# Kernel tuning notes

Hardware: AMD Instinct MI355X
Metric: run time of the kernel (lower is better)

The kernel has to match this reference:

```python
import jax, jax.numpy as jnp
import numpy as np


def setup_inputs() -> dict:
    key = jax.random.key(0)
    k1, k2 = jax.random.split(key)
    B, S, H, D = 2, 2048, 16, 64
    qk = jax.random.normal(k1, (B, S, 2, H, D), dtype=jnp.float32)
    v = jax.random.normal(k2, (B, S, H, D), dtype=jnp.float32)
    return {"qk": qk, "v": v}


def reference(qk, v):
    # qk: (B, S, 2, H, D); v: (B, S, H, D)
    seqlen = qk.shape[1]
    q = qk[:, :, 0]  # (B, S, H, D)
    k = qk[:, :, 1]
    # elu(x) + 1 feature map (positive features)
    q = jax.nn.elu(q) + 1.0
    k = jax.nn.elu(k) + 1.0
    # explicit O(S^2) score matrix: (B, H, T, S)
    scores = jnp.einsum('bthd,bshd->bhts', q, k)
    mask = jnp.tril(jnp.ones((seqlen, seqlen), dtype=scores.dtype))
    scores = scores * mask
    nu = scores.sum(axis=-1)  # (B, H, T)
    attention = scores / nu[:, :, :, None]
    # dropout_p = 0.0 (eval mode): identity
    output = jnp.einsum('bhts,bshd->bthd', attention, v)
    return output
```

## Files before the change

kernel.cpp:

```cpp
#include <hip/hip_runtime.h>


#define BB 2
#define SS 2048
#define HH 16
#define DD 64
#define CC 128
#define NC (SS / CC)
#define BH (BB * HH)
#define NCHUNK (BH * NC)
#define STSZ (DD * DD + DD)

#define WS_KB (512LL * 4160 * 4)
#define WS_VT (WS_KB + 512LL * 16384)
#define WS_S0 (WS_VT + 512LL * 16384)
#define WS_KZ (WS_S0 + 512LL * 8192)

typedef __attribute__((ext_vector_type(8))) short bf16x8;
typedef __attribute__((ext_vector_type(4))) float f32x4;

__device__ __forceinline__ float phi(float x) {
    return x > 0.f ? x + 1.f : __expf(x);
}
__device__ __forceinline__ unsigned short f2bf(float x) {
    unsigned int u = __float_as_uint(x);
    u += 0x7fffu + ((u >> 16) & 1u);
    return (unsigned short)(u >> 16);
}
__device__ __forceinline__ float bf2f(unsigned short b) {
    return __uint_as_float(((unsigned int)b) << 16);
}
__device__ __forceinline__ void gload16(const void* g, void* lds) {
    __builtin_amdgcn_global_load_lds(
        (const __attribute__((address_space(1))) unsigned int*)g,
        (__attribute__((address_space(3))) unsigned int*)lds, 16, 0, 0);
}

__global__ __launch_bounds__(256, 2)
void prep_state(const float* __restrict__ qk, const float* __restrict__ v,
                float* __restrict__ st, unsigned short* __restrict__ kbg,
                unsigned short* __restrict__ vtg) {
    __shared__ unsigned short Kt[DD][136];
    __shared__ unsigned short Vt[DD][136];

    const int tid = threadIdx.x, blk = blockIdx.x;
    const int bh = blk / NC, c = blk % NC, b = bh / HH, h = bh % HH;
    const int s0 = c * CC;
    const int lr = tid >> 4, lc = (tid & 15) * 4;
    char* kbc = (char*)kbg + (size_t)blk * 16384;

    #pragma unroll
    for (int it = 0; it < 8; ++it) {
        int row = it * 16 + lr;
        size_t ka = ((size_t)((b * SS + s0 + row) * 2 + 1)) * (HH * DD) + h * DD + lc;
        float4 kv = *(const float4*)(qk + ka);
        unsigned short k0 = f2bf(phi(kv.x)), k1 = f2bf(phi(kv.y));
        unsigned short k2 = f2bf(phi(kv.z)), k3 = f2bf(phi(kv.w));
        *(ushort4*)(kbc + row * 128 + ((lc * 2) ^ ((row & 7) << 4))) = make_ushort4(k0, k1, k2, k3);
        Kt[lc + 0][row] = k0; Kt[lc + 1][row] = k1;
        Kt[lc + 2][row] = k2; Kt[lc + 3][row] = k3;
        size_t va = ((size_t)((b * SS + s0 + row) * HH + h)) * DD + lc;
        float4 vv = *(const float4*)(v + va);
        Vt[lc + 0][row] = f2bf(vv.x); Vt[lc + 1][row] = f2bf(vv.y);
        Vt[lc + 2][row] = f2bf(vv.z); Vt[lc + 3][row] = f2bf(vv.w);
    }
    __syncthreads();

    {
        char* vtc = (char*)vtg + (size_t)blk * 16384;
        int e = tid >> 2, sq = (tid & 3) * 32;
        #pragma unroll
        for (int k8 = 0; k8 < 4; ++k8) {
            int s = sq + k8 * 8;
            bf16x8 val = *(const bf16x8*)&Vt[e][s];
            *(bf16x8*)(vtc + e * 256 + ((s * 2) ^ ((e & 7) << 4))) = val;
        }
    }

    const int w = tid >> 6, lane = tid & 63, g = lane >> 4, ln = lane & 15;
    bf16x8 av[4];
    #pragma unroll
    for (int ks = 0; ks < 4; ++ks)
        av[ks] = *(const bf16x8*)&Vt[w * 16 + ln][ks * 32 + g * 8];
    bf16x8 ones;
    #pragma unroll
    for (int j = 0; j < 8; ++j) ones[j] = (short)0x3F80;

    float* stc = st + (size_t)blk * STSZ;
    #pragma unroll
    for (int n = 0; n < 4; ++n) {
        f32x4 a = {0.f, 0.f, 0.f, 0.f}, kz4 = {0.f, 0.f, 0.f, 0.f};
        #pragma unroll
        for (int ks = 0; ks < 4; ++ks) {
            bf16x8 bk = *(const bf16x8*)&Kt[n * 16 + ln][ks * 32 + g * 8];
            a = __builtin_amdgcn_mfma_f32_16x16x32_bf16(av[ks], bk, a, 0, 0, 0);
            kz4 = __builtin_amdgcn_mfma_f32_16x16x32_bf16(ones, bk, kz4, 0, 0, 0);
        }
        #pragma unroll
        for (int r = 0; r < 4; ++r)
            stc[(w * 16 + g * 4 + r) * 64 + n * 16 + ln] = a[r];
        if (w == 0 && g == 0) stc[4096 + n * 16 + ln] = kz4[0];
    }
}

__global__ __launch_bounds__(256)
void chunk_scan(const float* __restrict__ st, unsigned short* __restrict__ s0g,
                float* __restrict__ kzg) {
    int flat = blockIdx.x * 256 + threadIdx.x;
    int bh = flat / 1040, i = flat % 1040;
    if (i < 1024) {
        int i4 = i * 4;
        int e = i4 >> 6, d = i4 & 63;
        const float* src = st + (size_t)(bh * NC) * STSZ + i4;
        char* dst = (char*)s0g + (size_t)(bh * NC) * 8192
                    + e * 128 + ((d * 2) ^ ((e & 7) << 4));
        float4 run = {0.f, 0.f, 0.f, 0.f};
        #pragma unroll
        for (int c2 = 0; c2 < NC; ++c2) {
            *(ushort4*)(dst + (size_t)c2 * 8192) =
                make_ushort4(f2bf(run.x), f2bf(run.y), f2bf(run.z), f2bf(run.w));
            float4 x = *(const float4*)(src + (size_t)c2 * STSZ);
            run.x += x.x; run.y += x.y; run.z += x.z; run.w += x.w;
        }
    } else {
        int j = (i - 1024) * 4;
        const float* src = st + (size_t)(bh * NC) * STSZ + 4096 + j;
        float* dst = kzg + (size_t)(bh * NC) * 64 + j;
        float4 run = {0.f, 0.f, 0.f, 0.f};
        #pragma unroll
        for (int c2 = 0; c2 < NC; ++c2) {
            *(float4*)(dst + (size_t)c2 * 64) = run;
            float4 x = *(const float4*)(src + (size_t)c2 * STSZ);
            run.x += x.x; run.y += x.y; run.z += x.z; run.w += x.w;
        }
    }
}

__global__ __launch_bounds__(256, 2)
void lin_attn_out(const float* __restrict__ qk,
                  const unsigned short* __restrict__ kbg,
                  const unsigned short* __restrict__ vtg,
                  const unsigned short* __restrict__ s0g,
                  const float* __restrict__ kzg,
                  float* __restrict__ out) {
    __shared__ __align__(16) char KbL[16384];
    __shared__ __align__(16) char VtL[16384];
    __shared__ __align__(16) char S0L[8192];
    __shared__ float kzl[DD];
    __shared__ __align__(16) unsigned short Wl[4][32][40];
    __shared__ float nul[4][32];

    const int tid = threadIdx.x, blk = blockIdx.x;
    const int bh = blk / NC, c = blk % NC, b = bh / HH, h = bh % HH;
    const int s0 = c * CC;
    const int w = tid >> 6, lane = tid & 63, g = lane >> 4, ln = lane & 15;

    {
        const char* kbs = (const char*)kbg + (size_t)blk * 16384;
        const char* vts = (const char*)vtg + (size_t)blk * 16384;
        const char* s0s = (const char*)s0g + (size_t)blk * 8192;
        #pragma unroll
        for (int i = 0; i < 4; ++i) {
            gload16(kbs + w * 4096 + i * 1024 + lane * 16, KbL + w * 4096 + i * 1024);
            gload16(vts + w * 4096 + i * 1024 + lane * 16, VtL + w * 4096 + i * 1024);
        }
        #pragma unroll
        for (int i = 0; i < 2; ++i)
            gload16(s0s + w * 2048 + i * 1024 + lane * 16, S0L + w * 2048 + i * 1024);
        if (tid < DD) kzl[tid] = kzg[(size_t)blk * 64 + tid];
    }

    bf16x8 aq[2][2];
    #pragma unroll
    for (int m = 0; m < 2; ++m) {
        int tg = s0 + w * 32 + m * 16 + ln;
        const float* qrow = qk + ((size_t)((b * SS + tg) * 2)) * (HH * DD) + h * DD;
        #pragma unroll
        for (int kb2 = 0; kb2 < 2; ++kb2) {
            float4 x0 = *(const float4*)(qrow + kb2 * 32 + g * 8);
            float4 x1 = *(const float4*)(qrow + kb2 * 32 + g * 8 + 4);
            bf16x8 f;
            f[0] = (short)f2bf(phi(x0.x)); f[1] = (short)f2bf(phi(x0.y));
            f[2] = (short)f2bf(phi(x0.z)); f[3] = (short)f2bf(phi(x0.w));
            f[4] = (short)f2bf(phi(x1.x)); f[5] = (short)f2bf(phi(x1.y));
            f[6] = (short)f2bf(phi(x1.z)); f[7] = (short)f2bf(phi(x1.w));
            aq[m][kb2] = f;
        }
    }
    __syncthreads();

    f32x4 O[2][4];
    #pragma unroll
    for (int m = 0; m < 2; ++m)
        #pragma unroll
        for (int n = 0; n < 4; ++n) O[m][n] = (f32x4){0.f, 0.f, 0.f, 0.f};

    #pragma unroll
    for (int n = 0; n < 4; ++n) {
        int e = n * 16 + ln;
        bf16x8 b0 = *(const bf16x8*)(S0L + e * 128 + ((g * 16) ^ ((e & 7) << 4)));
        bf16x8 b1 = *(const bf16x8*)(S0L + e * 128 + ((64 + g * 16) ^ ((e & 7) << 4)));
        #pragma unroll
        for (int m = 0; m < 2; ++m) {
            O[m][n] = __builtin_amdgcn_mfma_f32_16x16x32_bf16(aq[m][0], b0, O[m][n], 0, 0, 0);
            O[m][n] = __builtin_amdgcn_mfma_f32_16x16x32_bf16(aq[m][1], b1, O[m][n], 0, 0, 0);
        }
    }

    float nuA[2] = {0.f, 0.f};
    #pragma unroll
    for (int kb2 = 0; kb2 < 2; ++kb2)
        #pragma unroll
        for (int j = 0; j < 8; ++j) {
            float kzv = kzl[kb2 * 32 + g * 8 + j];
            nuA[0] = fmaf(bf2f((unsigned short)aq[0][kb2][j]), kzv, nuA[0]);
            nuA[1] = fmaf(bf2f((unsigned short)aq[1][kb2][j]), kzv, nuA[1]);
        }

    for (int sblk = 0; sblk <= w; ++sblk) {
        const bool diag = (sblk == w);
        f32x4 Sc[2][2];
        #pragma unroll
        for (int m = 0; m < 2; ++m)
            #pragma unroll
            for (int ns = 0; ns < 2; ++ns) Sc[m][ns] = (f32x4){0.f, 0.f, 0.f, 0.f};

        #pragma unroll
        for (int ns = 0; ns < 2; ++ns) {
            int s = sblk * 32 + ns * 16 + ln;
            const char* srow = KbL + s * 128;
            bf16x8 bk0 = *(const bf16x8*)(srow + ((g * 16) ^ ((s & 7) << 4)));
            bf16x8 bk1 = *(const bf16x8*)(srow + ((64 + g * 16) ^ ((s & 7) << 4)));
            #pragma unroll
            for (int m = 0; m < 2; ++m) {
                Sc[m][ns] = __builtin_amdgcn_mfma_f32_16x16x32_bf16(aq[m][0], bk0, Sc[m][ns], 0, 0, 0);
                Sc[m][ns] = __builtin_amdgcn_mfma_f32_16x16x32_bf16(aq[m][1], bk1, Sc[m][ns], 0, 0, 0);
            }
        }

        #pragma unroll
        for (int m = 0; m < 2; ++m)
            #pragma unroll
            for (int ns = 0; ns < 2; ++ns)
                #pragma unroll
                for (int r = 0; r < 4; ++r) {
                    int t_loc = m * 16 + g * 4 + r;
                    int s_loc = ns * 16 + ln;
                    float val = Sc[m][ns][r];
                    if (diag && s_loc > t_loc) val = 0.f;
                    Wl[w][t_loc][s_loc] = f2bf(val);
                }
        asm volatile("s_waitcnt lgkmcnt(0)" ::: "memory");
        __builtin_amdgcn_sched_barrier(0);

        bf16x8 bv[4];
        #pragma unroll
        for (int n = 0; n < 4; ++n) {
            int e = n * 16 + ln;
            bv[n] = *(const bf16x8*)(VtL + e * 256 + ((sblk * 64 + g * 16) ^ ((e & 7) << 4)));
        }

        #pragma unroll
        for (int m = 0; m < 2; ++m) {
            bf16x8 pa = *(const bf16x8*)&Wl[w][m * 16 + ln][g * 8];
            float rs = 0.f;
            #pragma unroll
            for (int j = 0; j < 8; ++j) rs += bf2f((unsigned short)pa[j]);
            nuA[m] += rs;
            #pragma unroll
            for (int n = 0; n < 4; ++n)
                O[m][n] = __builtin_amdgcn_mfma_f32_16x16x32_bf16(pa, bv[n], O[m][n], 0, 0, 0);
        }
    }

    #pragma unroll
    for (int m = 0; m < 2; ++m) {
        float nt = nuA[m];
        nt += __shfl_xor(nt, 16);
        nt += __shfl_xor(nt, 32);
        if (g == 0) nul[w][m * 16 + ln] = nt;
    }
    asm volatile("s_waitcnt lgkmcnt(0)" ::: "memory");
    __builtin_amdgcn_sched_barrier(0);

    #pragma unroll
    for (int m = 0; m < 2; ++m) {
        float inv[4];
        #pragma unroll
        for (int r = 0; r < 4; ++r) inv[r] = 1.f / nul[w][m * 16 + g * 4 + r];
        #pragma unroll
        for (int n = 0; n < 4; ++n)
            #pragma unroll
            for (int r = 0; r < 4; ++r) {
                int t = w * 32 + m * 16 + g * 4 + r;
                int e = n * 16 + ln;
                size_t oa = ((size_t)((b * SS + s0 + t) * HH + h)) * DD + e;
                out[oa] = O[m][n][r] * inv[r];
            }
    }
}

extern "C" void kernel_launch(void* const* d_in, const int* in_sizes, int n_in,
                              void* d_out, int out_size, void* d_ws, size_t ws_size,
                              hipStream_t stream) {
    const float* qk = (const float*)d_in[0];
    const float* v  = (const float*)d_in[1];
    float* outp = (float*)d_out;

    float* st = (float*)d_ws;
    unsigned short* kbg = (unsigned short*)((char*)d_ws + WS_KB);
    unsigned short* vtg = (unsigned short*)((char*)d_ws + WS_VT);
    unsigned short* s0g = (unsigned short*)((char*)d_ws + WS_S0);
    float* kzg = (float*)((char*)d_ws + WS_KZ);

    prep_state<<<NCHUNK, 256, 0, stream>>>(qk, v, st, kbg, vtg);
    chunk_scan<<<130, 256, 0, stream>>>(st, s0g, kzg);
    lin_attn_out<<<NCHUNK, 256, 0, stream>>>(qk, kbg, vtg, s0g, kzg, outp);
}
```

Baseline: 33.66 us.

## Fuse chunk scan into prep kernel via last-block ticket, store states in bf16

Removes the separate chunk_scan launch. Each prep_state block increments a per-head atomic ticket, and the last block to finish for that head runs the prefix scan over all chunk states. Per-chunk KV states are now stored as bf16 instead of fp32 to cut write and read traffic, and the ones-MFMA for the k sum runs only in wave 0. In lin_attn_out, odd blocks reverse their wave-to-band mapping to spread the causal triangle work more evenly. The cost is an extra memset launch, atomics and threadfences, a serialized scan tail on one block per head, and lower-precision state accumulation.

```diff
diff --git a/kernel.cpp b/kernel.cpp
--- a/kernel.cpp
+++ b/kernel.cpp
@@ -9,12 +9,13 @@
 #define NC (SS / CC)
 #define BH (BB * HH)
 #define NCHUNK (BH * NC)
-#define STSZ (DD * DD + DD)
-
-#define WS_KB (512LL * 4160 * 4)
+
+#define ST_STRIDE 8448LL
+#define WS_KB (512LL * ST_STRIDE)
 #define WS_VT (WS_KB + 512LL * 16384)
 #define WS_S0 (WS_VT + 512LL * 16384)
 #define WS_KZ (WS_S0 + 512LL * 8192)
+#define WS_TK (WS_KZ + 512LL * 256)
 
 typedef __attribute__((ext_vector_type(8))) short bf16x8;
 typedef __attribute__((ext_vector_type(4))) float f32x4;
@@ -38,10 +39,12 @@
 
 __global__ __launch_bounds__(256, 2)
 void prep_state(const float* __restrict__ qk, const float* __restrict__ v,
-                float* __restrict__ st, unsigned short* __restrict__ kbg,
-                unsigned short* __restrict__ vtg) {
+                char* __restrict__ st, unsigned short* __restrict__ kbg,
+                unsigned short* __restrict__ vtg, unsigned short* __restrict__ s0g,
+                float* __restrict__ kzg, int* __restrict__ tickets) {
     __shared__ unsigned short Kt[DD][136];
     __shared__ unsigned short Vt[DD][136];
+    __shared__ int lastflag;
 
     const int tid = threadIdx.x, blk = blockIdx.x;
     const int bh = blk / NC, c = blk % NC, b = bh / HH, h = bh % HH;
@@ -54,11 +57,11 @@
         int row = it * 16 + lr;
         size_t ka = ((size_t)((b * SS + s0 + row) * 2 + 1)) * (HH * DD) + h * DD + lc;
         float4 kv = *(const float4*)(qk + ka);
-        unsigned short k0 = f2bf(phi(kv.x)), k1 = f2bf(phi(kv.y));
-        unsigned short k2 = f2bf(phi(kv.z)), k3 = f2bf(phi(kv.w));
-        *(ushort4*)(kbc + row * 128 + ((lc * 2) ^ ((row & 7) << 4))) = make_ushort4(k0, k1, k2, k3);
-        Kt[lc + 0][row] = k0; Kt[lc + 1][row] = k1;
-        Kt[lc + 2][row] = k2; Kt[lc + 3][row] = k3;
+        ushort4 kq = make_ushort4(f2bf(phi(kv.x)), f2bf(phi(kv.y)),
+                                  f2bf(phi(kv.z)), f2bf(phi(kv.w)));
+        *(ushort4*)(kbc + row * 128 + ((lc * 2) ^ ((row & 7) << 4))) = kq;
+        Kt[lc + 0][row] = kq.x; Kt[lc + 1][row] = kq.y;
+        Kt[lc + 2][row] = kq.z; Kt[lc + 3][row] = kq.w;
         size_t va = ((size_t)((b * SS + s0 + row) * HH + h)) * DD + lc;
         float4 vv = *(const float4*)(v + va);
         Vt[lc + 0][row] = f2bf(vv.x); Vt[lc + 1][row] = f2bf(vv.y);
@@ -78,59 +81,71 @@
     }
 
     const int w = tid >> 6, lane = tid & 63, g = lane >> 4, ln = lane & 15;
-    bf16x8 av[4];
-    #pragma unroll
-    for (int ks = 0; ks < 4; ++ks)
-        av[ks] = *(const bf16x8*)&Vt[w * 16 + ln][ks * 32 + g * 8];
-    bf16x8 ones;
-    #pragma unroll
-    for (int j = 0; j < 8; ++j) ones[j] = (short)0x3F80;
-
-    float* stc = st + (size_t)blk * STSZ;
-    #pragma unroll
-    for (int n = 0; n < 4; ++n) {
-        f32x4 a = {0.f, 0.f, 0.f, 0.f}, kz4 = {0.f, 0.f, 0.f, 0.f};
-        #pragma unroll
-        for (int ks = 0; ks < 4; ++ks) {
-            bf16x8 bk = *(const bf16x8*)&Kt[n * 16 + ln][ks * 32 + g * 8];
-            a = __builtin_amdgcn_mfma_f32_16x16x32_bf16(av[ks], bk, a, 0, 0, 0);
-            kz4 = __builtin_amdgcn_mfma_f32_16x16x32_bf16(ones, bk, kz4, 0, 0, 0);
-        }
-        #pragma unroll
-        for (int r = 0; r < 4; ++r)
-            stc[(w * 16 + g * 4 + r) * 64 + n * 16 + ln] = a[r];
-        if (w == 0 && g == 0) stc[4096 + n * 16 + ln] = kz4[0];
-    }
-}
-
-__global__ __launch_bounds__(256)
-void chunk_scan(const float* __restrict__ st, unsigned short* __restrict__ s0g,
-                float* __restrict__ kzg) {
-    int flat = blockIdx.x * 256 + threadIdx.x;
-    int bh = flat / 1040, i = flat % 1040;
-    if (i < 1024) {
-        int i4 = i * 4;
-        int e = i4 >> 6, d = i4 & 63;
-        const float* src = st + (size_t)(bh * NC) * STSZ + i4;
-        char* dst = (char*)s0g + (size_t)(bh * NC) * 8192
-                    + e * 128 + ((d * 2) ^ ((e & 7) << 4));
+    {
+        bf16x8 av[4];
+        #pragma unroll
+        for (int ks = 0; ks < 4; ++ks)
+            av[ks] = *(const bf16x8*)&Vt[w * 16 + ln][ks * 32 + g * 8];
+        bf16x8 ones;
+        #pragma unroll
+        for (int j = 0; j < 8; ++j) ones[j] = (short)0x3F80;
+
+        char* stc = st + (size_t)blk * ST_STRIDE;
+        #pragma unroll
+        for (int n = 0; n < 4; ++n) {
+            f32x4 a = {0.f, 0.f, 0.f, 0.f}, kz4 = {0.f, 0.f, 0.f, 0.f};
+            #pragma unroll
+            for (int ks = 0; ks < 4; ++ks) {
+                bf16x8 bk = *(const bf16x8*)&Kt[n * 16 + ln][ks * 32 + g * 8];
+                a = __builtin_amdgcn_mfma_f32_16x16x32_bf16(av[ks], bk, a, 0, 0, 0);
+                if (w == 0)
+                    kz4 = __builtin_amdgcn_mfma_f32_16x16x32_bf16(ones, bk, kz4, 0, 0, 0);
+            }
+            #pragma unroll
+            for (int r = 0; r < 4; ++r)
+                *(unsigned short*)(stc + (((w * 16 + g * 4 + r) * 64) + n * 16 + ln) * 2)
+                    = f2bf(a[r]);
+            if (w == 0 && g == 0)
+                *(float*)(stc + 8192 + (n * 16 + ln) * 4) = kz4[0];
+        }
+    }
+
+    __threadfence();
+    __syncthreads();
+    if (tid == 0)
+        lastflag = (atomicAdd(&tickets[bh], 1) == NC - 1) ? 1 : 0;
+    __syncthreads();
+    if (!lastflag) return;
+    __threadfence();
+
+    const char* stb = st + (size_t)(bh * NC) * ST_STRIDE;
+    char* s0b = (char*)s0g + (size_t)(bh * NC) * 8192;
+    float* kzb = kzg + (size_t)(bh * NC) * 64;
+    #pragma unroll
+    for (int it = 0; it < 4; ++it) {
+        int i = it * 256 + tid;
+        int i4 = i * 4, e = i4 >> 6, d = i4 & 63;
+        const char* src = stb + i * 8;
+        char* dst = s0b + e * 128 + ((d * 2) ^ ((e & 7) << 4));
         float4 run = {0.f, 0.f, 0.f, 0.f};
         #pragma unroll
         for (int c2 = 0; c2 < NC; ++c2) {
             *(ushort4*)(dst + (size_t)c2 * 8192) =
                 make_ushort4(f2bf(run.x), f2bf(run.y), f2bf(run.z), f2bf(run.w));
-            float4 x = *(const float4*)(src + (size_t)c2 * STSZ);
-            run.x += x.x; run.y += x.y; run.z += x.z; run.w += x.w;
-        }
-    } else {
-        int j = (i - 1024) * 4;
-        const float* src = st + (size_t)(bh * NC) * STSZ + 4096 + j;
-        float* dst = kzg + (size_t)(bh * NC) * 64 + j;
+            ushort4 x = *(const ushort4*)(src + (size_t)c2 * ST_STRIDE);
+            run.x += bf2f(x.x); run.y += bf2f(x.y);
+            run.z += bf2f(x.z); run.w += bf2f(x.w);
+        }
+    }
+    if (tid < 16) {
+        int j = tid * 4;
+        const char* src = stb + 8192 + j * 4;
+        float* dst = kzb + j;
         float4 run = {0.f, 0.f, 0.f, 0.f};
         #pragma unroll
         for (int c2 = 0; c2 < NC; ++c2) {
             *(float4*)(dst + (size_t)c2 * 64) = run;
-            float4 x = *(const float4*)(src + (size_t)c2 * STSZ);
+            float4 x = *(const float4*)(src + (size_t)c2 * ST_STRIDE);
             run.x += x.x; run.y += x.y; run.z += x.z; run.w += x.w;
         }
     }
@@ -154,6 +169,7 @@
     const int bh = blk / NC, c = blk % NC, b = bh / HH, h = bh % HH;
     const int s0 = c * CC;
     const int w = tid >> 6, lane = tid & 63, g = lane >> 4, ln = lane & 15;
+    const int wband = (blk & 1) ? (3 - w) : w;
 
     {
         const char* kbs = (const char*)kbg + (size_t)blk * 16384;
@@ -173,7 +189,7 @@
     bf16x8 aq[2][2];
     #pragma unroll
     for (int m = 0; m < 2; ++m) {
-        int tg = s0 + w * 32 + m * 16 + ln;
+        int tg = s0 + wband * 32 + m * 16 + ln;
         const float* qrow = qk + ((size_t)((b * SS + tg) * 2)) * (HH * DD) + h * DD;
         #pragma unroll
         for (int kb2 = 0; kb2 < 2; ++kb2) {
@@ -217,8 +233,8 @@
             nuA[1] = fmaf(bf2f((unsigned short)aq[1][kb2][j]), kzv, nuA[1]);
         }
 
-    for (int sblk = 0; sblk <= w; ++sblk) {
-        const bool diag = (sblk == w);
+    for (int sblk = 0; sblk <= wband; ++sblk) {
+        const bool diag = (sblk == wband);
         f32x4 Sc[2][2];
         #pragma unroll
         for (int m = 0; m < 2; ++m)
@@ -292,7 +308,7 @@
         for (int n = 0; n < 4; ++n)
             #pragma unroll
             for (int r = 0; r < 4; ++r) {
-                int t = w * 32 + m * 16 + g * 4 + r;
+                int t = wband * 32 + m * 16 + g * 4 + r;
                 int e = n * 16 + ln;
                 size_t oa = ((size_t)((b * SS + s0 + t) * HH + h)) * DD + e;
                 out[oa] = O[m][n][r] * inv[r];
@@ -307,13 +323,14 @@
     const float* v  = (const float*)d_in[1];
     float* outp = (float*)d_out;
 
-    float* st = (float*)d_ws;
+    char* st = (char*)d_ws;
     unsigned short* kbg = (unsigned short*)((char*)d_ws + WS_KB);
     unsigned short* vtg = (unsigned short*)((char*)d_ws + WS_VT);
     unsigned short* s0g = (unsigned short*)((char*)d_ws + WS_S0);
     float* kzg = (float*)((char*)d_ws + WS_KZ);
-
-    prep_state<<<NCHUNK, 256, 0, stream>>>(qk, v, st, kbg, vtg);
-    chunk_scan<<<130, 256, 0, stream>>>(st, s0g, kzg);
+    int* tickets = (int*)((char*)d_ws + WS_TK);
+
+    hipMemsetAsync(tickets, 0, BH * sizeof(int), stream);
+    prep_state<<<NCHUNK, 256, 0, stream>>>(qk, v, st, kbg, vtg, s0g, kzg, tickets);
     lin_attn_out<<<NCHUNK, 256, 0, stream>>>(qk, kbg, vtg, s0g, kzg, outp);
 }
```

Result: slower. 115.3 us (+242.4%).

## Split output kernel chunks into two half-blocks, 16 query rows per wave

Applied to the files above, without the earlier changes.

The output kernel now launches twice as many blocks. Each block handles half of a 128-row chunk, so each wave processes 16 query rows instead of 32. Occupancy is raised to 3 blocks per CU, and the causal work per wave is rebalanced. This adds parallelism and better load balance across the 256 CUs. In exchange, each chunk's K, V and S0 tiles are loaded into LDS twice, which doubles that global traffic.

```diff
diff --git a/kernel.cpp b/kernel.cpp
--- a/kernel.cpp
+++ b/kernel.cpp
@@ -17,6 +17,7 @@
 #define WS_KZ (WS_S0 + 512LL * 8192)
 
 typedef __attribute__((ext_vector_type(8))) short bf16x8;
+typedef __attribute__((ext_vector_type(4))) short bf16x4;
 typedef __attribute__((ext_vector_type(4))) float f32x4;
 
 __device__ __forceinline__ float phi(float x) {
@@ -86,7 +87,7 @@
     #pragma unroll
     for (int j = 0; j < 8; ++j) ones[j] = (short)0x3F80;
 
-    float* stc = st + (size_t)blk * STSZ;
+    float* o = st + (size_t)blk * STSZ;
     #pragma unroll
     for (int n = 0; n < 4; ++n) {
         f32x4 a = {0.f, 0.f, 0.f, 0.f}, kz4 = {0.f, 0.f, 0.f, 0.f};
@@ -98,8 +99,8 @@
         }
         #pragma unroll
         for (int r = 0; r < 4; ++r)
-            stc[(w * 16 + g * 4 + r) * 64 + n * 16 + ln] = a[r];
-        if (w == 0 && g == 0) stc[4096 + n * 16 + ln] = kz4[0];
+            o[(w * 16 + g * 4 + r) * 64 + n * 16 + ln] = a[r];
+        if (w == 0 && g == 0) o[4096 + n * 16 + ln] = kz4[0];
     }
 }
 
@@ -136,7 +137,7 @@
     }
 }
 
-__global__ __launch_bounds__(256, 2)
+__global__ __launch_bounds__(256, 3)
 void lin_attn_out(const float* __restrict__ qk,
                   const unsigned short* __restrict__ kbg,
                   const unsigned short* __restrict__ vtg,
@@ -147,18 +148,22 @@
     __shared__ __align__(16) char VtL[16384];
     __shared__ __align__(16) char S0L[8192];
     __shared__ float kzl[DD];
-    __shared__ __align__(16) unsigned short Wl[4][32][40];
-    __shared__ float nul[4][32];
+    __shared__ __align__(16) unsigned short Wl[4][16][40];
+    __shared__ float nul[4][16];
 
     const int tid = threadIdx.x, blk = blockIdx.x;
-    const int bh = blk / NC, c = blk % NC, b = bh / HH, h = bh % HH;
+    const int bh = blk >> 5, hc = blk & 31;
+    const int c = hc >> 1, half = hc & 1;
+    const int b = bh / HH, h = bh % HH;
     const int s0 = c * CC;
+    const int ck = bh * NC + c;
     const int w = tid >> 6, lane = tid & 63, g = lane >> 4, ln = lane & 15;
-
-    {
-        const char* kbs = (const char*)kbg + (size_t)blk * 16384;
-        const char* vts = (const char*)vtg + (size_t)blk * 16384;
-        const char* s0s = (const char*)s0g + (size_t)blk * 8192;
+    const int T0 = half * 64 + w * 16;
+
+    {
+        const char* kbs = (const char*)kbg + (size_t)ck * 16384;
+        const char* vts = (const char*)vtg + (size_t)ck * 16384;
+        const char* s0s = (const char*)s0g + (size_t)ck * 8192;
         #pragma unroll
         for (int i = 0; i < 4; ++i) {
             gload16(kbs + w * 4096 + i * 1024 + lane * 16, KbL + w * 4096 + i * 1024);
@@ -167,13 +172,12 @@
         #pragma unroll
         for (int i = 0; i < 2; ++i)
             gload16(s0s + w * 2048 + i * 1024 + lane * 16, S0L + w * 2048 + i * 1024);
-        if (tid < DD) kzl[tid] = kzg[(size_t)blk * 64 + tid];
-    }
-
-    bf16x8 aq[2][2];
-    #pragma unroll
-    for (int m = 0; m < 2; ++m) {
-        int tg = s0 + w * 32 + m * 16 + ln;
+        if (tid < DD) kzl[tid] = kzg[(size_t)ck * 64 + tid];
+    }
+
+    bf16x8 aq[2];
+    {
+        int tg = s0 + T0 + ln;
         const float* qrow = qk + ((size_t)((b * SS + tg) * 2)) * (HH * DD) + h * DD;
         #pragma unroll
         for (int kb2 = 0; kb2 < 2; ++kb2) {
@@ -184,72 +188,58 @@
             f[2] = (short)f2bf(phi(x0.z)); f[3] = (short)f2bf(phi(x0.w));
             f[4] = (short)f2bf(phi(x1.x)); f[5] = (short)f2bf(phi(x1.y));
             f[6] = (short)f2bf(phi(x1.z)); f[7] = (short)f2bf(phi(x1.w));
-            aq[m][kb2] = f;
+            aq[kb2] = f;
         }
     }
     __syncthreads();
 
-    f32x4 O[2][4];
-    #pragma unroll
-    for (int m = 0; m < 2; ++m)
-        #pragma unroll
-        for (int n = 0; n < 4; ++n) O[m][n] = (f32x4){0.f, 0.f, 0.f, 0.f};
+    f32x4 O[4];
+    #pragma unroll
+    for (int n = 0; n < 4; ++n) O[n] = (f32x4){0.f, 0.f, 0.f, 0.f};
 
     #pragma unroll
     for (int n = 0; n < 4; ++n) {
         int e = n * 16 + ln;
         bf16x8 b0 = *(const bf16x8*)(S0L + e * 128 + ((g * 16) ^ ((e & 7) << 4)));
         bf16x8 b1 = *(const bf16x8*)(S0L + e * 128 + ((64 + g * 16) ^ ((e & 7) << 4)));
-        #pragma unroll
-        for (int m = 0; m < 2; ++m) {
-            O[m][n] = __builtin_amdgcn_mfma_f32_16x16x32_bf16(aq[m][0], b0, O[m][n], 0, 0, 0);
-            O[m][n] = __builtin_amdgcn_mfma_f32_16x16x32_bf16(aq[m][1], b1, O[m][n], 0, 0, 0);
-        }
-    }
-
-    float nuA[2] = {0.f, 0.f};
+        O[n] = __builtin_amdgcn_mfma_f32_16x16x32_bf16(aq[0], b0, O[n], 0, 0, 0);
+        O[n] = __builtin_amdgcn_mfma_f32_16x16x32_bf16(aq[1], b1, O[n], 0, 0, 0);
+    }
+
+    float nuA = 0.f;
     #pragma unroll
     for (int kb2 = 0; kb2 < 2; ++kb2)
         #pragma unroll
-        for (int j = 0; j < 8; ++j) {
-            float kzv = kzl[kb2 * 32 + g * 8 + j];
-            nuA[0] = fmaf(bf2f((unsigned short)aq[0][kb2][j]), kzv, nuA[0]);
-            nuA[1] = fmaf(bf2f((unsigned short)aq[1][kb2][j]), kzv, nuA[1]);
-        }
-
-    for (int sblk = 0; sblk <= w; ++sblk) {
-        const bool diag = (sblk == w);
-        f32x4 Sc[2][2];
-        #pragma unroll
-        for (int m = 0; m < 2; ++m)
-            #pragma unroll
-            for (int ns = 0; ns < 2; ++ns) Sc[m][ns] = (f32x4){0.f, 0.f, 0.f, 0.f};
+        for (int j = 0; j < 8; ++j)
+            nuA = fmaf(bf2f((unsigned short)aq[kb2][j]), kzl[kb2 * 32 + g * 8 + j], nuA);
+
+    const int dsb = T0 >> 5;
+    for (int sb = 0; sb <= dsb; ++sb) {
+        const bool diag = (sb == dsb);
+        f32x4 Sc[2];
+        #pragma unroll
+        for (int ns = 0; ns < 2; ++ns) Sc[ns] = (f32x4){0.f, 0.f, 0.f, 0.f};
 
         #pragma unroll
         for (int ns = 0; ns < 2; ++ns) {
-            int s = sblk * 32 + ns * 16 + ln;
+            int s = sb * 32 + ns * 16 + ln;
             const char* srow = KbL + s * 128;
             bf16x8 bk0 = *(const bf16x8*)(srow + ((g * 16) ^ ((s & 7) << 4)));
             bf16x8 bk1 = *(const bf16x8*)(srow + ((64 + g * 16) ^ ((s & 7) << 4)));
+            Sc[ns] = __builtin_amdgcn_mfma_f32_16x16x32_bf16(aq[0], bk0, Sc[ns], 0, 0, 0);
+            Sc[ns] = __builtin_amdgcn_mfma_f32_16x16x32_bf16(aq[1], bk1, Sc[ns], 0, 0, 0);
+        }
+
+        #pragma unroll
+        for (int ns = 0; ns < 2; ++ns)
             #pragma unroll
-            for (int m = 0; m < 2; ++m) {
-                Sc[m][ns] = __builtin_amdgcn_mfma_f32_16x16x32_bf16(aq[m][0], bk0, Sc[m][ns], 0, 0, 0);
-                Sc[m][ns] = __builtin_amdgcn_mfma_f32_16x16x32_bf16(aq[m][1], bk1, Sc[m][ns], 0, 0, 0);
+            for (int r = 0; r < 4; ++r) {
+                int t_cr = T0 + g * 4 + r;
+                int s_cr = sb * 32 + ns * 16 + ln;
+                float val = Sc[ns][r];
+                if (diag && s_cr > t_cr) val = 0.f;
+                Wl[w][g * 4 + r][ns * 16 + ln] = f2bf(val);
             }
-        }
-
-        #pragma unroll
-        for (int m = 0; m < 2; ++m)
-            #pragma unroll
-            for (int ns = 0; ns < 2; ++ns)
-                #pragma unroll
-                for (int r = 0; r < 4; ++r) {
-                    int t_loc = m * 16 + g * 4 + r;
-                    int s_loc = ns * 16 + ln;
-                    float val = Sc[m][ns][r];
-                    if (diag && s_loc > t_loc) val = 0.f;
-                    Wl[w][t_loc][s_loc] = f2bf(val);
-                }
         asm volatile("s_waitcnt lgkmcnt(0)" ::: "memory");
         __builtin_amdgcn_sched_barrier(0);
 
@@ -257,45 +247,45 @@
         #pragma unroll
         for (int n = 0; n < 4; ++n) {
             int e = n * 16 + ln;
-            bv[n] = *(const bf16x8*)(VtL + e * 256 + ((sblk * 64 + g * 16) ^ ((e & 7) << 4)));
-        }
-
-        #pragma unroll
-        for (int m = 0; m < 2; ++m) {
-            bf16x8 pa = *(const bf16x8*)&Wl[w][m * 16 + ln][g * 8];
+            bv[n] = *(const bf16x8*)(VtL + e * 256 + ((sb * 64 + g * 16) ^ ((e & 7) << 4)));
+        }
+
+        {
+            const unsigned short* prow = &Wl[w][ln][0];
+            bf16x4 plo = *(const bf16x4*)(prow + g * 8);
+            bf16x4 phi2 = *(const bf16x4*)(prow + g * 8 + 4);
+            bf16x8 pa = __builtin_shufflevector(plo, phi2, 0, 1, 2, 3, 4, 5, 6, 7);
             float rs = 0.f;
             #pragma unroll
             for (int j = 0; j < 8; ++j) rs += bf2f((unsigned short)pa[j]);
-            nuA[m] += rs;
+            nuA += rs;
             #pragma unroll
             for (int n = 0; n < 4; ++n)
-                O[m][n] = __builtin_amdgcn_mfma_f32_16x16x32_bf16(pa, bv[n], O[m][n], 0, 0, 0);
-        }
-    }
-
-    #pragma unroll
-    for (int m = 0; m < 2; ++m) {
-        float nt = nuA[m];
+                O[n] = __builtin_amdgcn_mfma_f32_16x16x32_bf16(pa, bv[n], O[n], 0, 0, 0);
+        }
+    }
+
+    {
+        float nt = nuA;
         nt += __shfl_xor(nt, 16);
         nt += __shfl_xor(nt, 32);
-        if (g == 0) nul[w][m * 16 + ln] = nt;
+        if (g == 0) nul[w][ln] = nt;
     }
     asm volatile("s_waitcnt lgkmcnt(0)" ::: "memory");
     __builtin_amdgcn_sched_barrier(0);
 
-    #pragma unroll
-    for (int m = 0; m < 2; ++m) {
+    {
         float inv[4];
         #pragma unroll
-        for (int r = 0; r < 4; ++r) inv[r] = 1.f / nul[w][m * 16 + g * 4 + r];
+        for (int r = 0; r < 4; ++r) inv[r] = 1.f / nul[w][g * 4 + r];
         #pragma unroll
         for (int n = 0; n < 4; ++n)
             #pragma unroll
             for (int r = 0; r < 4; ++r) {
-                int t = w * 32 + m * 16 + g * 4 + r;
+                int t = T0 + g * 4 + r;
                 int e = n * 16 + ln;
                 size_t oa = ((size_t)((b * SS + s0 + t) * HH + h)) * DD + e;
-                out[oa] = O[m][n][r] * inv[r];
+                out[oa] = O[n][r] * inv[r];
             }
     }
 }
@@ -315,5 +305,5 @@
 
     prep_state<<<NCHUNK, 256, 0, stream>>>(qk, v, st, kbg, vtg);
     chunk_scan<<<130, 256, 0, stream>>>(st, s0g, kzg);
-    lin_attn_out<<<NCHUNK, 256, 0, stream>>>(qk, kbg, vtg, s0g, kzg, outp);
-}
+    lin_attn_out<<<NCHUNK * 2, 256, 0, stream>>>(qk, kbg, vtg, s0g, kzg, outp);
+}
```

Measured after the change: 36.32 us. +7.9%, slower.
